# Optimization experiments

Measured on AMD Instinct MI355X. Metric: run time of the kernel, lower is better.

## Reference

```python
import jax, jax.numpy as jnp
import numpy as np

EPS = 1e-6

def _rms_norm(x, w):
    # torch: x / (||x||_2 * n^{-1/2} + eps) * w
    rms = jnp.linalg.norm(x, axis=-1, keepdims=True) * (x.shape[-1] ** -0.5)
    return x / (rms + EPS) * w

def _rope_cos_sin(seq_len, head_dim):
    half = head_dim // 2
    freq = 1.0 / (10000.0 ** (jnp.arange(half, dtype=jnp.float32) / half))
    t = jnp.arange(seq_len, dtype=jnp.float32)
    freqs = t[:, None] * freq[None, :]            # [s, half]
    freqs = jnp.concatenate([freqs, freqs], -1)   # [s, d_head]
    cos = jnp.cos(freqs)[None, :, None, :]        # [1, s, 1, d_head]
    sin = jnp.sin(freqs)[None, :, None, :]
    return cos, sin

def _rotate_half(x):
    h = x.shape[-1] // 2
    return jnp.concatenate([-x[..., h:], x[..., :h]], -1)

def setup_inputs() -> dict:
    key = jax.random.key(0)
    ks = jax.random.split(key, 8)
    B, S, D, H, F = 2, 2048, 2048, 16, 128
    return {
        'query_input': jax.random.normal(ks[0], (B, S, D), jnp.float32),
        'key_input':   jax.random.normal(ks[1], (B, S, D), jnp.float32),
        'value_input': jax.random.normal(ks[2], (B, S, D), jnp.float32),
        'W_Q': jax.random.normal(ks[3], (H, D, F), jnp.float32) * (D ** -0.5),
        'W_K': jax.random.normal(ks[4], (H, D, F), jnp.float32) * (D ** -0.5),
        'W_V': jax.random.normal(ks[5], (H, D, F), jnp.float32) * (D ** -0.5),
        'W_O': jax.random.normal(ks[6], (H, F, D), jnp.float32) * (F ** -0.5),
        'b_Q': jnp.zeros((H, F), jnp.float32),
        'b_K': jnp.zeros((H, F), jnp.float32),
        'b_V': jnp.zeros((H, F), jnp.float32),
        'b_O': jnp.zeros((D,), jnp.float32),
        'q_norm_w': jnp.ones((F,), jnp.float32),
        'k_norm_w': jnp.ones((F,), jnp.float32),
    }

def reference(query_input, key_input, value_input, W_Q, W_K, W_V, W_O,
              b_Q, b_K, b_V, b_O, q_norm_w, k_norm_w):
    head_dim = W_Q.shape[-1]
    q = jnp.einsum('bpd,hdf->bphf', query_input, W_Q) + b_Q[None, None]
    k = jnp.einsum('bpd,hdf->bphf', key_input,   W_K) + b_K[None, None]
    v = jnp.einsum('bpd,hdf->bphf', value_input, W_V) + b_V[None, None]
    q = _rms_norm(q, q_norm_w)
    k = _rms_norm(k, k_norm_w)
    cos, sin = _rope_cos_sin(q.shape[1], head_dim)
    q = q * cos + _rotate_half(q) * sin
    k = k * cos + _rotate_half(k) * sin
    scores = jnp.einsum('bphf,bqhf->bhpq', q, k) / (head_dim ** 0.5)
    pattern = jax.nn.softmax(scores, axis=-1)
    attn = jnp.einsum('bhpq,bqhf->bphf', pattern, v)
    return jnp.einsum('bphf,hfm->bpm', attn, W_O) + b_O
```

## Files before the change

### kernel.cpp

```cpp
#include <hip/hip_runtime.h>
#include <stdint.h>

typedef unsigned short u16;
typedef __attribute__((ext_vector_type(8))) short  s8b;
typedef __attribute__((ext_vector_type(4))) float  f32x4;

#define S_LEN   2048
#define NHEAD   16
#define HD      128
#define DM      2048
#define NB      2
#define NPLANE  (NB*NHEAD)
#define ROWS    (NB*S_LEN)
#define PLANE_ELEMS (S_LEN*HD)
#define ATT_SCALE 0.08838834764831845f
#define LOG2E     1.4426950408889634f

__device__ __forceinline__ float bf2f(u16 u){
  union { unsigned u; float f; } x; x.u = ((unsigned)u) << 16; return x.f;
}
__device__ __forceinline__ u16 f2bf(float f){
  union { float f; unsigned u; } x; x.f = f;
  unsigned r = x.u + 0x7FFFu + ((x.u >> 16) & 1u);
  return (u16)(r >> 16);
}
__device__ __forceinline__ unsigned cvtpk(float lo, float hi){
  unsigned r;
  asm("v_cvt_pk_bf16_f32 %0, %1, %2" : "=v"(r) : "v"(lo), "v"(hi));
  return r;
}

typedef const __attribute__((address_space(1))) unsigned int* gas1;
typedef __attribute__((address_space(3))) unsigned int* las3;
__device__ __forceinline__ void gload16(const void* g, void* l){
  __builtin_amdgcn_global_load_lds((gas1)g, (las3)l, 16, 0, 0);
}

__device__ __forceinline__ f32x4 mfma16(s8b a, s8b b, f32x4 c){
  return __builtin_amdgcn_mfma_f32_16x16x32_bf16(a, b, c, 0, 0, 0);
}

__global__ __launch_bounds__(256) void cvt4x3(const float4* __restrict__ a,
                                              const float4* __restrict__ b,
                                              const float4* __restrict__ c,
                                              uint2* __restrict__ oa,
                                              uint2* __restrict__ ob,
                                              uint2* __restrict__ oc, int n4){
  int i = blockIdx.x*256 + threadIdx.x;
  if (i >= n4) return;
  const float4* src = (blockIdx.y == 0) ? a : (blockIdx.y == 1) ? b : c;
  uint2*       dst  = (blockIdx.y == 0) ? oa : (blockIdx.y == 1) ? ob : oc;
  float4 v = src[i];
  uint2 o;
  o.x = (unsigned)f2bf(v.x) | ((unsigned)f2bf(v.y) << 16);
  o.y = (unsigned)f2bf(v.z) | ((unsigned)f2bf(v.w) << 16);
  dst[i] = o;
}

__global__ __launch_bounds__(256) void transpose_cvt(const float* __restrict__ in,
                                                     u16* __restrict__ out,
                                                     int R, int C, int outStride){
  __shared__ float tile[32][33];
  int z = blockIdx.z;
  const float* inz = in + (size_t)z * R * C;
  u16* outz = out + (size_t)z * C * outStride;
  int r0 = blockIdx.x*32, c0 = blockIdx.y*32;
  int tx = threadIdx.x, ty = threadIdx.y;
  #pragma unroll
  for (int i=0;i<4;i++)
    tile[ty*4+i][tx] = inz[(size_t)(r0+ty*4+i)*C + c0 + tx];
  __syncthreads();
  #pragma unroll
  for (int i=0;i<4;i++)
    outz[(size_t)(c0+ty*4+i)*outStride + r0 + tx] = f2bf(tile[tx][ty*4+i]);
}

__global__ __launch_bounds__(256) void rope_tab(float* __restrict__ ctab,
                                                float* __restrict__ stab){
  int i = blockIdx.x*256 + threadIdx.x;
  int p = i >> 6, j = i & 63;
  float freq = exp2f(-(float)j * (13.287712379549449f/64.0f));
  float a = (float)p * freq;
  ctab[i] = cosf(a);
  stab[i] = sinf(a);
}

__global__ __launch_bounds__(256) void gemm_bt(const u16* __restrict__ A,
                                               const u16* __restrict__ BT,
                                               const float* __restrict__ bias,
                                               void* __restrict__ out, int mode){
  const int K = 2048;
  __shared__ u16 As[2][4096];
  __shared__ u16 Bs[2][4096];
  const int t = threadIdx.x, w = t >> 6, l = t & 63;
  const int lr = l & 15, lg = l >> 4;
  int bid = blockIdx.x;
  int swz = (bid & 7)*64 + (bid >> 3);
  const int M0 = (swz >> 4) * 128, N0 = (swz & 15) * 128;
  const int wr = w >> 1, wc = w & 1;

  f32x4 acc[4][4];
  #pragma unroll
  for (int i=0;i<4;i++)
    #pragma unroll
    for (int j=0;j<4;j++) acc[i][j] = f32x4{0.f,0.f,0.f,0.f};

  auto stage = [&](int buf, int kt){
    #pragma unroll
    for (int c=0;c<2;c++){
      int mloc = c*64 + w*16 + (l>>2);
      int kloc = (l&3)*8;
      gload16(A  + (size_t)(M0+mloc)*K + kt*32 + kloc, &As[buf][c*2048 + w*512]);
      gload16(BT + (size_t)(N0+mloc)*K + kt*32 + kloc, &Bs[buf][c*2048 + w*512]);
    }
  };

  stage(0, 0);
  int cur = 0;
  const int NT = K/32;
  for (int kt=0; kt<NT; kt++){
    __syncthreads();
    if (kt+1 < NT) stage(cur^1, kt+1);
    s8b af[4], bf[4];
    #pragma unroll
    for (int i=0;i<4;i++){
      af[i] = *(const s8b*)&As[cur][(wr*64 + i*16 + lr)*32 + lg*8];
      bf[i] = *(const s8b*)&Bs[cur][(wc*64 + i*16 + lr)*32 + lg*8];
    }
    __builtin_amdgcn_s_setprio(1);
    #pragma unroll
    for (int i=0;i<4;i++)
      #pragma unroll
      for (int j=0;j<4;j++)
        acc[i][j] = mfma16(af[i], bf[j], acc[i][j]);
    __builtin_amdgcn_s_setprio(0);
    cur ^= 1;
  }

  #pragma unroll
  for (int i=0;i<4;i++){
    int growb = M0 + wr*64 + i*16 + lg*4;
    #pragma unroll
    for (int j=0;j<4;j++){
      int gcol = N0 + wc*64 + j*16 + lr;
      float bv = bias[gcol];
      #pragma unroll
      for (int r=0;r<4;r++){
        int grow = growb + r;
        float v = acc[i][j][r] + bv;
        if (mode == 2){
          ((float*)out)[(size_t)grow*2048 + gcol] = v;
        } else {
          int b = grow >> 11, p = grow & 2047;
          int h = gcol >> 7,  f = gcol & 127;
          if (mode == 0){
            ((u16*)out)[(((size_t)(b*NHEAD+h))*S_LEN + p)*HD + f] = f2bf(v);
          } else {
            size_t base = ((size_t)(b*NHEAD+h)*PLANE_ELEMS + (size_t)(p>>6)*8192) * 2;
            int p6 = p & 63;
            int q_ = ((p6&12)<<1) | (p6&3) | ((p6&16)>>2);
            int kvp = (p6 & 32) | q_;
            int byte = (f*128 + kvp*2) ^ ((f&7)<<4);
            *(u16*)((char*)out + base + byte) = f2bf(v);
          }
        }
      }
    }
  }
}

__global__ __launch_bounds__(256) void norm_rope(const u16* __restrict__ in,
                                                 u16* __restrict__ outp,
                                                 const float* __restrict__ nw,
                                                 const float* __restrict__ ctab,
                                                 const float* __restrict__ stab,
                                                 int swizzled, float oscale){
  int t = threadIdx.x, w = t>>6, l = t&63;
  size_t R = (size_t)blockIdx.x*4 + w;
  int p = (int)(R & (S_LEN-1));
  size_t base = R * HD;
  float x0 = bf2f(in[base + l]);
  float x1 = bf2f(in[base + 64 + l]);
  float ss = x0*x0 + x1*x1;
  #pragma unroll
  for (int m=1;m<64;m<<=1) ss += __shfl_xor(ss, m);
  float rms = sqrtf(ss * (1.0f/128.0f));
  float sc = oscale / (rms + 1e-6f);
  float xn0 = x0 * sc * nw[l];
  float xn1 = x1 * sc * nw[64+l];
  float c = ctab[(size_t)p*64 + l], s = stab[(size_t)p*64 + l];
  float o0 = xn0*c - xn1*s;
  float o1 = xn1*c + xn0*s;
  if (!swizzled){
    outp[base + l]      = f2bf(o0);
    outp[base + 64 + l] = f2bf(o1);
  } else {
    size_t plane = R >> 11;
    int kv = p & 63;
    size_t tb = (plane*(size_t)PLANE_ELEMS + (size_t)(p>>6)*8192) * 2;
    int b0 = (kv*256 + l*2)        ^ ((kv&7)<<4);
    int b1 = (kv*256 + (64+l)*2)   ^ ((kv&7)<<4);
    *(u16*)((char*)outp + tb + b0) = f2bf(o0);
    *(u16*)((char*)outp + tb + b1) = f2bf(o1);
  }
}

__global__ __launch_bounds__(256,2) void attn_fwd(const u16* __restrict__ qn,
                                                  const u16* __restrict__ kn,
                                                  const u16* __restrict__ vt,
                                                  u16* __restrict__ attn_out){
  __shared__ u16 Klds[2][8192];
  __shared__ u16 Vlds[2][8192];
  int t = threadIdx.x, w = t>>6, l = t&63;
  int lr = l&15, lg = l>>4;

  int bid = blockIdx.x;
  int xcd = bid & 7, j = bid >> 3;
  int plane = xcd*4 + (j >> 4);
  int qb = j & 15;
  int q0 = qb*128 + w*32;

  s8b qf[2][4];
  #pragma unroll
  for (int qi=0; qi<2; qi++)
    #pragma unroll
    for (int fc=0; fc<4; fc++)
      qf[qi][fc] = *(const s8b*)(qn + ((size_t)plane*S_LEN + q0 + qi*16 + lr)*HD + fc*32 + lg*8);

  float m[2], lsum[2];
  #pragma unroll
  for (int qi=0;qi<2;qi++){ m[qi] = -1e30f; lsum[qi] = 0.f; }
  f32x4 oacc[2][8];
  #pragma unroll
  for (int qi=0;qi<2;qi++)
    #pragma unroll
    for (int i=0;i<8;i++) oacc[qi][i] = f32x4{0.f,0.f,0.f,0.f};

  const u16* kbase = kn + (size_t)plane*PLANE_ELEMS;
  const u16* vbase = vt + (size_t)plane*PLANE_ELEMS;

  auto stage = [&](int buf, int kt){
    #pragma unroll
    for (int i=0;i<4;i++){
      gload16(kbase + (size_t)kt*8192 + w*2048 + i*512 + l*8, &Klds[buf][w*2048 + i*512]);
      gload16(vbase + (size_t)kt*8192 + w*2048 + i*512 + l*8, &Vlds[buf][w*2048 + i*512]);
    }
  };

  stage(0, 0);
  int cur = 0;
  for (int kt=0; kt<32; kt++){
    __syncthreads();
    if (kt+1 < 32) stage(cur^1, kt+1);

    f32x4 sacc[4][2];
    #pragma unroll
    for (int c=0;c<4;c++)
      #pragma unroll
      for (int qi=0;qi<2;qi++) sacc[c][qi] = f32x4{0.f,0.f,0.f,0.f};
    __builtin_amdgcn_s_setprio(1);
    #pragma unroll
    for (int c=0;c<4;c++){
      int kv = c*16 + lr;
      #pragma unroll
      for (int fc=0; fc<4; fc++){
        int byte = (kv*256 + (fc*32 + lg*8)*2) ^ ((kv&7)<<4);
        s8b kf = *(const s8b*)((const char*)&Klds[cur][0] + byte);
        sacc[c][0] = mfma16(kf, qf[0][fc], sacc[c][0]);
        sacc[c][1] = mfma16(kf, qf[1][fc], sacc[c][1]);
      }
    }
    __builtin_amdgcn_s_setprio(0);

    float mx[2];
    #pragma unroll
    for (int qi=0;qi<2;qi++){
      float a0 = fmaxf(fmaxf(sacc[0][qi][0], sacc[0][qi][1]), fmaxf(sacc[0][qi][2], sacc[0][qi][3]));
      float a1 = fmaxf(fmaxf(sacc[1][qi][0], sacc[1][qi][1]), fmaxf(sacc[1][qi][2], sacc[1][qi][3]));
      float a2 = fmaxf(fmaxf(sacc[2][qi][0], sacc[2][qi][1]), fmaxf(sacc[2][qi][2], sacc[2][qi][3]));
      float a3 = fmaxf(fmaxf(sacc[3][qi][0], sacc[3][qi][1]), fmaxf(sacc[3][qi][2], sacc[3][qi][3]));
      mx[qi] = fmaxf(fmaxf(a0, a1), fmaxf(a2, a3));
    }
    bool need = (mx[0] > m[0] + 11.5f) || (mx[1] > m[1] + 11.5f);
    if (__any(need)){
      #pragma unroll
      for (int qi=0;qi<2;qi++){
        float v = mx[qi];
        v = fmaxf(v, __shfl_xor(v, 16));
        v = fmaxf(v, __shfl_xor(v, 32));
        v = fmaxf(m[qi], v);
        float al = exp2f(m[qi] - v);
        m[qi] = v; lsum[qi] *= al;
        float alr[4];
        #pragma unroll
        for (int r=0;r<4;r++) alr[r] = __shfl(al, lg*4 + r);
        #pragma unroll
        for (int i=0;i<8;i++)
          #pragma unroll
          for (int r=0;r<4;r++) oacc[qi][i][r] *= alr[r];
      }
    }
    float pv[2][4][4];
    #pragma unroll
    for (int qi=0;qi<2;qi++){
      float ls0=0.f, ls1=0.f, ls2=0.f, ls3=0.f;
      #pragma unroll
      for (int c=0;c<4;c++){
        float e0 = exp2f(sacc[c][qi][0] - m[qi]);
        float e1 = exp2f(sacc[c][qi][1] - m[qi]);
        float e2 = exp2f(sacc[c][qi][2] - m[qi]);
        float e3 = exp2f(sacc[c][qi][3] - m[qi]);
        pv[qi][c][0]=e0; pv[qi][c][1]=e1; pv[qi][c][2]=e2; pv[qi][c][3]=e3;
        ls0 += e0; ls1 += e1; ls2 += e2; ls3 += e3;
      }
      lsum[qi] += (ls0 + ls1) + (ls2 + ls3);
    }

    s8b pa[2][2];
    #pragma unroll
    for (int qi=0;qi<2;qi++)
      #pragma unroll
      for (int kc=0;kc<2;kc++){
        union { s8b v; unsigned u[4]; } pu;
        pu.u[0] = cvtpk(pv[qi][2*kc][0],   pv[qi][2*kc][1]);
        pu.u[1] = cvtpk(pv[qi][2*kc][2],   pv[qi][2*kc][3]);
        pu.u[2] = cvtpk(pv[qi][2*kc+1][0], pv[qi][2*kc+1][1]);
        pu.u[3] = cvtpk(pv[qi][2*kc+1][2], pv[qi][2*kc+1][3]);
        pa[qi][kc] = pu.v;
      }

    __builtin_amdgcn_s_setprio(1);
    #pragma unroll
    for (int kc=0;kc<2;kc++){
      #pragma unroll
      for (int fc2=0; fc2<8; fc2++){
        int f = fc2*16 + lr;
        int byte = (f*128 + (kc*32 + lg*8)*2) ^ ((f&7)<<4);
        s8b vf = *(const s8b*)((const char*)&Vlds[cur][0] + byte);
        oacc[0][fc2] = mfma16(pa[0][kc], vf, oacc[0][fc2]);
        oacc[1][fc2] = mfma16(pa[1][kc], vf, oacc[1][fc2]);
      }
    }
    __builtin_amdgcn_s_setprio(0);
    cur ^= 1;
  }

  int b = plane >> 4, h = plane & 15;
  #pragma unroll
  for (int qi=0;qi<2;qi++){
    float v = lsum[qi];
    v += __shfl_xor(v, 16);
    v += __shfl_xor(v, 32);
    v = 1.0f / v;
    float lir[4];
    #pragma unroll
    for (int r=0;r<4;r++) lir[r] = __shfl(v, lg*4 + r);
    #pragma unroll
    for (int fc2=0; fc2<8; fc2++){
      int f = fc2*16 + lr;
      #pragma unroll
      for (int r=0;r<4;r++){
        int row = q0 + qi*16 + lg*4 + r;
        float o = oacc[qi][fc2][r] * lir[r];
        attn_out[(((size_t)b*S_LEN + row)*NHEAD + h)*HD + f] = f2bf(o);
      }
    }
  }
}

extern "C" void kernel_launch(void* const* d_in, const int* in_sizes, int n_in,
                              void* d_out, int out_size, void* d_ws, size_t ws_size,
                              hipStream_t stream){
  const float* xq = (const float*)d_in[0];
  const float* xk = (const float*)d_in[1];
  const float* xv = (const float*)d_in[2];
  const float* WQ = (const float*)d_in[3];
  const float* WK = (const float*)d_in[4];
  const float* WV = (const float*)d_in[5];
  const float* WO = (const float*)d_in[6];
  const float* bQ = (const float*)d_in[7];
  const float* bK = (const float*)d_in[8];
  const float* bV = (const float*)d_in[9];
  const float* bO = (const float*)d_in[10];
  const float* qw = (const float*)d_in[11];
  const float* kw = (const float*)d_in[12];

  char* ws = (char*)d_ws;
  size_t off = 0;
  auto alloc = [&](size_t bytes)->void*{
    void* p = ws + off; off += (bytes + 255) & ~(size_t)255; return p;
  };
  const size_t ACT = (size_t)ROWS*DM*2;
  const size_t WMT = (size_t)DM*DM*2;
  u16* xqb  = (u16*)alloc(ACT);
  u16* xkb  = (u16*)alloc(ACT);
  u16* xvb  = (u16*)alloc(ACT);
  u16* WqT  = (u16*)alloc(WMT);
  u16* WkT  = (u16*)alloc(WMT);
  u16* WvT  = (u16*)alloc(WMT);
  u16* WoT  = (u16*)alloc(WMT);
  u16* qraw = (u16*)alloc(ACT);
  u16* kraw = (u16*)alloc(ACT);
  u16* knT  = (u16*)alloc(ACT);
  u16* vtS  = (u16*)alloc(ACT);
  u16* attn = (u16*)alloc(ACT);
  float* ctab = (float*)alloc((size_t)S_LEN*64*4);
  float* stab = (float*)alloc((size_t)S_LEN*64*4);
  if (off > ws_size) return;

  const int n4 = ROWS*DM/4;
  cvt4x3<<<dim3(n4/256, 3), dim3(256), 0, stream>>>((const float4*)xq, (const float4*)xk,
                                                    (const float4*)xv, (uint2*)xqb,
                                                    (uint2*)xkb, (uint2*)xvb, n4);
  rope_tab<<<dim3(S_LEN*64/256), dim3(256), 0, stream>>>(ctab, stab);
  transpose_cvt<<<dim3(64,4,16), dim3(32,8), 0, stream>>>(WQ, WqT, 2048, 128, 2048);
  transpose_cvt<<<dim3(64,4,16), dim3(32,8), 0, stream>>>(WK, WkT, 2048, 128, 2048);
  transpose_cvt<<<dim3(64,4,16), dim3(32,8), 0, stream>>>(WV, WvT, 2048, 128, 2048);
  transpose_cvt<<<dim3(64,64,1), dim3(32,8), 0, stream>>>(WO, WoT, 2048, 2048, 2048);

  gemm_bt<<<dim3(512), dim3(256), 0, stream>>>(xqb, WqT, bQ, qraw, 0);
  gemm_bt<<<dim3(512), dim3(256), 0, stream>>>(xkb, WkT, bK, kraw, 0);
  gemm_bt<<<dim3(512), dim3(256), 0, stream>>>(xvb, WvT, bV, vtS, 1);

  norm_rope<<<dim3(NPLANE*S_LEN/4), dim3(256), 0, stream>>>(qraw, qraw, qw, ctab, stab, 0, ATT_SCALE*LOG2E);
  norm_rope<<<dim3(NPLANE*S_LEN/4), dim3(256), 0, stream>>>(kraw, knT, kw, ctab, stab, 1, 1.0f);

  attn_fwd<<<dim3(512), dim3(256), 0, stream>>>(qraw, knT, vtS, attn);

  gemm_bt<<<dim3(512), dim3(256), 0, stream>>>(attn, WoT, bO, d_out, 2);
}
```

Baseline: 375.7 us.

## Rewrite projection GEMM with 256x128 tiles, 512 threads, triple-buffered swizzled LDS

The bf16 GEMM used for the Q/K/V and output projections moves from 128x128 tiles with 256 threads and a double-buffered K=32 pipeline to 256x128 tiles with 512 threads and K=64 steps. It stages half-tiles into a six-slot LDS ring with an XOR swizzle and keeps two k-steps in flight using explicit vmcnt waits and split barriers. The goals are better data reuse per block, fewer LDS bank conflicts, and more overlap of global loads with MFMA work. In exchange it uses much more LDS, about 144KB per block, so occupancy is limited, and the grid shrinks to 256 blocks. The hand-tuned waitcnt and barrier schedule is also fragile.

```diff
diff --git a/kernel.cpp b/kernel.cpp
--- a/kernel.cpp
+++ b/kernel.cpp
@@ -85,19 +85,19 @@
   stab[i] = sinf(a);
 }
 
-__global__ __launch_bounds__(256) void gemm_bt(const u16* __restrict__ A,
+__global__ __launch_bounds__(512) void gemm_bt(const u16* __restrict__ A,
                                                const u16* __restrict__ BT,
                                                const float* __restrict__ bias,
                                                void* __restrict__ out, int mode){
   const int K = 2048;
-  __shared__ u16 As[2][4096];
-  __shared__ u16 Bs[2][4096];
+  const int NT = 32;
+  __shared__ u16 lds[6*12288];
   const int t = threadIdx.x, w = t >> 6, l = t & 63;
   const int lr = l & 15, lg = l >> 4;
+  const int wr = w >> 1, wc = w & 1;
   int bid = blockIdx.x;
-  int swz = (bid & 7)*64 + (bid >> 3);
-  const int M0 = (swz >> 4) * 128, N0 = (swz & 15) * 128;
-  const int wr = w >> 1, wc = w & 1;
+  int swz = (bid & 7)*32 + (bid >> 3);
+  const int M0 = (swz >> 4) * 256, N0 = (swz & 15) * 128;
 
   f32x4 acc[4][4];
   #pragma unroll
@@ -105,49 +105,119 @@
     #pragma unroll
     for (int j=0;j<4;j++) acc[i][j] = f32x4{0.f,0.f,0.f,0.f};
 
-  auto stage = [&](int buf, int kt){
-    #pragma unroll
-    for (int c=0;c<2;c++){
-      int mloc = c*64 + w*16 + (l>>2);
-      int kloc = (l&3)*8;
-      gload16(A  + (size_t)(M0+mloc)*K + kt*32 + kloc, &As[buf][c*2048 + w*512]);
-      gload16(BT + (size_t)(N0+mloc)*K + kt*32 + kloc, &Bs[buf][c*2048 + w*512]);
+  auto stageH = [&](int ttu, int h){
+    int slot = (2*ttu + h) % 6;
+    int tt   = ttu & 31;
+    char* base = (char*)&lds[slot*12288];
+    #pragma unroll
+    for (int j=0;j<2;j++){
+      int d = w*2048 + j*1024 + l*16;
+      int row = d >> 7;
+      int koff = ((l&7)*16) ^ ((row&7)<<4);
+      gload16((const char*)A + ((size_t)(M0 + h*128 + row)*K + tt*64)*2 + koff,
+              base + w*2048 + j*1024);
+    }
+    {
+      int d = w*1024 + l*16;
+      int row = d >> 7;
+      int koff = ((l&7)*16) ^ ((row&7)<<4);
+      gload16((const char*)BT + ((size_t)(N0 + h*64 + row)*K + tt*64)*2 + koff,
+              base + 16384 + w*1024);
     }
   };
 
-  stage(0, 0);
-  int cur = 0;
-  const int NT = K/32;
+  stageH(0,0); stageH(0,1); stageH(1,0); stageH(1,1);
+
   for (int kt=0; kt<NT; kt++){
-    __syncthreads();
-    if (kt+1 < NT) stage(cur^1, kt+1);
-    s8b af[4], bf[4];
-    #pragma unroll
-    for (int i=0;i<4;i++){
-      af[i] = *(const s8b*)&As[cur][(wr*64 + i*16 + lr)*32 + lg*8];
-      bf[i] = *(const s8b*)&Bs[cur][(wc*64 + i*16 + lr)*32 + lg*8];
-    }
-    __builtin_amdgcn_s_setprio(1);
-    #pragma unroll
-    for (int i=0;i<4;i++)
-      #pragma unroll
-      for (int j=0;j<4;j++)
-        acc[i][j] = mfma16(af[i], bf[j], acc[i][j]);
-    __builtin_amdgcn_s_setprio(0);
-    cur ^= 1;
+    const char* Ab = (const char*)&lds[((2*kt + (wr>>1)) % 6)*12288];
+    const char* Bb = (const char*)&lds[((2*kt + wc) % 6)*12288] + 16384;
+
+    stageH(kt+2, 0);
+    asm volatile("s_waitcnt vmcnt(9)" ::: "memory");
+    __builtin_amdgcn_s_barrier();
+    __builtin_amdgcn_sched_barrier(0);
+
+    s8b af[4][2];
+    #pragma unroll
+    for (int mi=0;mi<4;mi++)
+      #pragma unroll
+      for (int kc=0;kc<2;kc++){
+        int rA = (wr&1)*64 + mi*16 + lr;
+        af[mi][kc] = *(const s8b*)(Ab + rA*128 + ((kc*64 + lg*16) ^ ((rA&7)<<4)));
+      }
+    {
+      s8b bf0, bf1;
+      int rB = 0*16 + lr;
+      bf0 = *(const s8b*)(Bb + rB*128 + ((0*64 + lg*16) ^ ((rB&7)<<4)));
+      bf1 = *(const s8b*)(Bb + rB*128 + ((1*64 + lg*16) ^ ((rB&7)<<4)));
+      __builtin_amdgcn_s_setprio(1);
+      #pragma unroll
+      for (int mi=0;mi<4;mi++){
+        acc[mi][0] = mfma16(af[mi][0], bf0, acc[mi][0]);
+        acc[mi][0] = mfma16(af[mi][1], bf1, acc[mi][0]);
+      }
+      __builtin_amdgcn_s_setprio(0);
+    }
+    {
+      s8b bf0, bf1;
+      int rB = 1*16 + lr;
+      bf0 = *(const s8b*)(Bb + rB*128 + ((0*64 + lg*16) ^ ((rB&7)<<4)));
+      bf1 = *(const s8b*)(Bb + rB*128 + ((1*64 + lg*16) ^ ((rB&7)<<4)));
+      __builtin_amdgcn_s_setprio(1);
+      #pragma unroll
+      for (int mi=0;mi<4;mi++){
+        acc[mi][1] = mfma16(af[mi][0], bf0, acc[mi][1]);
+        acc[mi][1] = mfma16(af[mi][1], bf1, acc[mi][1]);
+      }
+      __builtin_amdgcn_s_setprio(0);
+    }
+    __builtin_amdgcn_sched_barrier(0);
+    __builtin_amdgcn_s_barrier();
+    __builtin_amdgcn_sched_barrier(0);
+    stageH(kt+2, 1);
+    {
+      s8b bf0, bf1;
+      int rB = 2*16 + lr;
+      bf0 = *(const s8b*)(Bb + rB*128 + ((0*64 + lg*16) ^ ((rB&7)<<4)));
+      bf1 = *(const s8b*)(Bb + rB*128 + ((1*64 + lg*16) ^ ((rB&7)<<4)));
+      __builtin_amdgcn_s_setprio(1);
+      #pragma unroll
+      for (int mi=0;mi<4;mi++){
+        acc[mi][2] = mfma16(af[mi][0], bf0, acc[mi][2]);
+        acc[mi][2] = mfma16(af[mi][1], bf1, acc[mi][2]);
+      }
+      __builtin_amdgcn_s_setprio(0);
+    }
+    {
+      s8b bf0, bf1;
+      int rB = 3*16 + lr;
+      bf0 = *(const s8b*)(Bb + rB*128 + ((0*64 + lg*16) ^ ((rB&7)<<4)));
+      bf1 = *(const s8b*)(Bb + rB*128 + ((1*64 + lg*16) ^ ((rB&7)<<4)));
+      __builtin_amdgcn_s_setprio(1);
+      #pragma unroll
+      for (int mi=0;mi<4;mi++){
+        acc[mi][3] = mfma16(af[mi][0], bf0, acc[mi][3]);
+        acc[mi][3] = mfma16(af[mi][1], bf1, acc[mi][3]);
+      }
+      __builtin_amdgcn_s_setprio(0);
+    }
+    __builtin_amdgcn_sched_barrier(0);
+    __builtin_amdgcn_s_barrier();
+    __builtin_amdgcn_sched_barrier(0);
   }
-
-  #pragma unroll
-  for (int i=0;i<4;i++){
-    int growb = M0 + wr*64 + i*16 + lg*4;
-    #pragma unroll
-    for (int j=0;j<4;j++){
-      int gcol = N0 + wc*64 + j*16 + lr;
+  asm volatile("s_waitcnt vmcnt(0)" ::: "memory");
+
+  #pragma unroll
+  for (int mi=0;mi<4;mi++){
+    int growb = M0 + wr*64 + mi*16 + lg*4;
+    #pragma unroll
+    for (int nj=0;nj<4;nj++){
+      int gcol = N0 + wc*64 + nj*16 + lr;
       float bv = bias[gcol];
       #pragma unroll
       for (int r=0;r<4;r++){
         int grow = growb + r;
-        float v = acc[i][j][r] + bv;
+        float v = acc[mi][nj][r] + bv;
         if (mode == 2){
           ((float*)out)[(size_t)grow*2048 + gcol] = v;
         } else {
@@ -418,14 +488,14 @@
   transpose_cvt<<<dim3(64,4,16), dim3(32,8), 0, stream>>>(WV, WvT, 2048, 128, 2048);
   transpose_cvt<<<dim3(64,64,1), dim3(32,8), 0, stream>>>(WO, WoT, 2048, 2048, 2048);
 
-  gemm_bt<<<dim3(512), dim3(256), 0, stream>>>(xqb, WqT, bQ, qraw, 0);
-  gemm_bt<<<dim3(512), dim3(256), 0, stream>>>(xkb, WkT, bK, kraw, 0);
-  gemm_bt<<<dim3(512), dim3(256), 0, stream>>>(xvb, WvT, bV, vtS, 1);
+  gemm_bt<<<dim3(256), dim3(512), 0, stream>>>(xqb, WqT, bQ, qraw, 0);
+  gemm_bt<<<dim3(256), dim3(512), 0, stream>>>(xkb, WkT, bK, kraw, 0);
+  gemm_bt<<<dim3(256), dim3(512), 0, stream>>>(xvb, WvT, bV, vtS, 1);
 
   norm_rope<<<dim3(NPLANE*S_LEN/4), dim3(256), 0, stream>>>(qraw, qraw, qw, ctab, stab, 0, ATT_SCALE*LOG2E);
   norm_rope<<<dim3(NPLANE*S_LEN/4), dim3(256), 0, stream>>>(kraw, knT, kw, ctab, stab, 1, 1.0f);
 
   attn_fwd<<<dim3(512), dim3(256), 0, stream>>>(qraw, knT, vtS, attn);
 
-  gemm_bt<<<dim3(512), dim3(256), 0, stream>>>(attn, WoT, bO, d_out, 2);
-}
+  gemm_bt<<<dim3(256), dim3(512), 0, stream>>>(attn, WoT, bO, d_out, 2);
+}
```

Result: faster. 352.1 us (-6.3%).
